# Kernel optimization log

Measured on AMD Instinct MI355X. Metric: run time of the kernel, lower is better.

The kernel has to match this reference:

```python
import jax, jax.numpy as jnp
import numpy as np

C = 32          # middle_channels
N_DOWN = 13     # layers 2..14, stride 2
DENSITY = 0.01  # nnz fraction of the 2048x2048 sparse matrix


def _conv(x, w):
    # centered SAME conv; inactive sites hold zeros so they contribute nothing,
    # matching MinkowskiConvolution's sum over existing neighbor coordinates.
    return jax.lax.conv_general_dilated(
        x, w, window_strides=(1, 1), padding='SAME',
        dimension_numbers=('NHWC', 'HWIO', 'NHWC'))


def _downsample_mask(mask):
    # ME stride-2 output coords = stride-quantized input coords -> OR over 2x2 block
    return jax.lax.reduce_window(mask, 0.0, jax.lax.max, (1, 2, 2), (1, 2, 2), 'SAME')


def _layer(x, mask, w, stride):
    y = _conv(x, w)
    if stride > 1:
        y = y[:, ::stride, ::stride, :]   # value at quantized coordinate u
        mask = _downsample_mask(mask)
    y = jax.nn.relu(y) * mask[..., None]  # ReLU on active sites, keep inactive = 0
    return y, mask


def _global_avg_pool(x, mask):
    cnt = jnp.maximum(jnp.sum(mask, axis=(1, 2)), 1.0)  # number of active coords
    return jnp.sum(x, axis=(1, 2)) / cnt[:, None]       # [B, C]


def setup_inputs() -> dict:
    key = jax.random.key(0)
    ks = jax.random.split(key, 8)
    H = W = 2048
    mask = (jax.random.uniform(ks[0], (1, H, W)) < DENSITY).astype(jnp.float32)
    x = jax.random.normal(ks[1], (1, H, W, 1), dtype=jnp.float32) * mask[..., None]
    # kaiming_normal fan_out (nonlinearity='relu') for conv kernels, bias=False in ME
    w1 = jax.random.normal(ks[2], (5, 5, 1, C), dtype=jnp.float32) * np.float32((2.0 / (5 * 5 * C)) ** 0.5)
    ws = jax.random.normal(ks[3], (N_DOWN, 3, 3, C, C), dtype=jnp.float32) * np.float32((2.0 / (3 * 3 * C)) ** 0.5)
    wm1 = jax.random.normal(ks[4], (C * 14, 256), dtype=jnp.float32) * np.float32((1.0 / (C * 14)) ** 0.5)
    bm1 = jnp.zeros((256,), jnp.float32)
    wm2 = jax.random.normal(ks[5], (256, 128), dtype=jnp.float32) * np.float32((1.0 / 256) ** 0.5)
    bm2 = jnp.zeros((128,), jnp.float32)
    return {'x': x, 'mask': mask, 'w1': w1, 'ws': ws,
            'wm1': wm1, 'bm1': bm1, 'wm2': wm2, 'bm2': bm2}


def reference(x, mask, w1, ws, wm1, bm1, wm2, bm2):
    y, m = _layer(x, mask, w1, stride=1)          # layer1: k=5, s=1
    pools = [_global_avg_pool(y, m)]
    for i in range(N_DOWN):                       # layers 2..14: k=3, s=2
        y, m = _layer(y, m, ws[i], stride=2)
        pools.append(_global_avg_pool(y, m))
    feat = jnp.concatenate(pools, axis=-1)        # [B, 32*14]
    h = jax.nn.relu(feat @ wm1 + bm1)
    return h @ wm2 + bm2                          # [B, 128]
```

## Files before the change

### kernel.cpp

```cpp
#include <hip/hip_runtime.h>

#define NLVL 14
#define NSHARD 16

struct ZeroArgs { unsigned long long zoff[13]; };

struct TailArgs {
    char* ws;
    const float* wm1; const float* bm1;
    const float* wm2; const float* bm2;
    float* out;
    unsigned long long idx8, idx9, idx10;
    unsigned long long nbr8, nbr9, nbr10;
    unsigned long long val7, val8, val9;
    int cap8, cap9, cap10;
};

__device__ __forceinline__ float fma4(float4 v, float4 w, float acc) {
    acc = fmaf(v.x, w.x, acc);
    acc = fmaf(v.y, w.y, acc);
    acc = fmaf(v.z, w.z, acc);
    return fmaf(v.w, w.w, acc);
}

__device__ __forceinline__ int cnt_load(const int* p) {
    return __hip_atomic_load(p, __ATOMIC_RELAXED, __HIP_MEMORY_SCOPE_AGENT);
}

#define GLDS16(gsrc, ldst) __builtin_amdgcn_global_load_lds( \
    (const __attribute__((address_space(1))) void*)(gsrc),   \
    (__attribute__((address_space(3))) void*)(ldst), 16, 0, 0)

__device__ __forceinline__ int block_scan_base(int mycnt, int* gcnt, int& myoff) {
    __shared__ int wsum[4];
    __shared__ int base;
    __syncthreads();
    int lane = threadIdx.x & 63, wid = threadIdx.x >> 6;
    int scan = mycnt;
    #pragma unroll
    for (int d = 1; d < 64; d <<= 1) {
        int tv = __shfl_up(scan, d, 64);
        if (lane >= d) scan += tv;
    }
    if (lane == 63) wsum[wid] = scan;
    __syncthreads();
    if (threadIdx.x == 0) {
        int tot = 0;
        #pragma unroll
        for (int i = 0; i < 4; i++) { int tv = wsum[i]; wsum[i] = tot; tot += tv; }
        base = tot ? atomicAdd(gcnt, tot) : 0;
    }
    __syncthreads();
    myoff = wsum[wid] + scan - mycnt;
    return base;
}

__device__ void compact0_tile(const float4* __restrict__ mask4, int* __restrict__ idxmap,
                              int* __restrict__ coords, int* __restrict__ cnt, int cap, int tile) {
    int t = threadIdx.x;
    int g0 = tile * 1024 + t;
    float4 m[4];
    #pragma unroll
    for (int j = 0; j < 4; j++) m[j] = mask4[g0 + j * 256];
    int pr[16];
    int mycnt = 0;
    #pragma unroll
    for (int j = 0; j < 4; j++) {
        pr[4 * j + 0] = m[j].x > 0.5f;
        pr[4 * j + 1] = m[j].y > 0.5f;
        pr[4 * j + 2] = m[j].z > 0.5f;
        pr[4 * j + 3] = m[j].w > 0.5f;
        mycnt += pr[4 * j] + pr[4 * j + 1] + pr[4 * j + 2] + pr[4 * j + 3];
    }
    int myoff;
    int base = block_scan_base(mycnt, cnt, myoff);
    int slot = base + myoff;
    #pragma unroll
    for (int j = 0; j < 4; j++) {
        int e0 = (g0 + j * 256) << 2;
        int wv[4];
        #pragma unroll
        for (int k = 0; k < 4; k++) {
            wv[k] = -1;
            if (pr[4 * j + k]) {
                int sl = slot++;
                if (sl < cap) { wv[k] = sl; coords[sl] = e0 + k; }
            }
        }
        *(int4*)(idxmap + e0) = make_int4(wv[0], wv[1], wv[2], wv[3]);
    }
}

__device__ void down_nbr(const int* __restrict__ idx_in, int HinB,
                         int* __restrict__ idx_out, int* __restrict__ nbr_out,
                         int* __restrict__ cnt_out, int HoutB, int cap_out,
                         int zofs, int bb) {
    int Hout = 1 << HoutB, Hin = 1 << HinB;
    int S = Hout * Hout;
    int S4 = (S + 3) >> 2;
    int o4 = bb * 256 + threadIdx.x;
    int e0 = o4 << 2;
    int jv[4][9];
    int pr[4] = {0, 0, 0, 0};
    #pragma unroll
    for (int k = 0; k < 4; k++)
        #pragma unroll
        for (int tap = 0; tap < 9; tap++) jv[k][tap] = -1;
    if (o4 < S4) {
        if (HoutB >= 2) {
            int r = e0 >> HoutB, c0 = e0 & (Hout - 1);
            int w[3][12];
            #pragma unroll
            for (int a = 0; a < 3; a++) {
                int rr = 2 * r + a - 1;
                bool rok = (unsigned)rr < (unsigned)Hin;
                const int* rowp = idx_in + ((size_t)(rok ? rr : 0) << HinB) + 2 * c0;
                int4 L = (rok && c0 > 0) ? *(const int4*)(rowp - 4) : make_int4(-1, -1, -1, -1);
                int4 M = rok ? *(const int4*)rowp : make_int4(-1, -1, -1, -1);
                int4 R = rok ? *(const int4*)(rowp + 4) : make_int4(-1, -1, -1, -1);
                w[a][0] = L.x; w[a][1] = L.y; w[a][2]  = L.z; w[a][3]  = L.w;
                w[a][4] = M.x; w[a][5] = M.y; w[a][6]  = M.z; w[a][7]  = M.w;
                w[a][8] = R.x; w[a][9] = R.y; w[a][10] = R.z; w[a][11] = R.w;
            }
            #pragma unroll
            for (int k = 0; k < 4; k++) {
                #pragma unroll
                for (int a = 0; a < 3; a++)
                    #pragma unroll
                    for (int b = 0; b < 3; b++)
                        jv[k][a * 3 + b] = w[a][2 * k + b + 3];
                pr[k] = ((jv[k][4] & jv[k][5] & jv[k][7] & jv[k][8]) >= 0);
            }
        } else {
            #pragma unroll
            for (int k = 0; k < 4; k++) {
                int p = e0 + k;
                if (p < S) {
                    int r = p >> HoutB, c = p & (Hout - 1);
                    #pragma unroll
                    for (int a = 0; a < 3; a++)
                        #pragma unroll
                        for (int b = 0; b < 3; b++) {
                            int rr = 2 * r + a - 1, cc = 2 * c + b - 1;
                            if ((unsigned)rr < (unsigned)Hin && (unsigned)cc < (unsigned)Hin)
                                jv[k][a * 3 + b] = idx_in[((size_t)rr << HinB) + cc];
                        }
                    pr[k] = ((jv[k][4] & jv[k][5] & jv[k][7] & jv[k][8]) >= 0);
                }
            }
        }
    }
    int mycnt = pr[0] + pr[1] + pr[2] + pr[3];
    int myoff;
    int base = block_scan_base(mycnt, cnt_out, myoff);
    int slot = base + myoff;
    int wv[4] = {-1, -1, -1, -1};
    #pragma unroll
    for (int k = 0; k < 4; k++) {
        if (pr[k]) {
            int sl = slot++;
            if (sl < cap_out) {
                wv[k] = sl;
                #pragma unroll
                for (int tap = 0; tap < 9; tap++) {
                    int j = jv[k][tap];
                    nbr_out[sl * 9 + tap] = (j < 0) ? zofs : (j << 7);
                }
            }
        }
    }
    if (o4 < S4) {
        if (S >= 4) *(int4*)(idx_out + e0) = make_int4(wv[0], wv[1], wv[2], wv[3]);
        else {
            #pragma unroll
            for (int k = 0; k < 4; k++) if (e0 + k < S) idx_out[e0 + k] = wv[k];
        }
    }
}

__device__ void down_small_wave(const int* __restrict__ idx_in, int HinB,
                                int* __restrict__ idx_out, int* __restrict__ nbr_out,
                                int* __restrict__ cnt_out, int HoutB, int cap_out,
                                int zofs) {
    int t = threadIdx.x;
    int Hout = 1 << HoutB, Hin = 1 << HinB, S = Hout * Hout;
    int p = t;
    int jv[9];
    int pr = 0;
    #pragma unroll
    for (int tap = 0; tap < 9; tap++) jv[tap] = -1;
    if (p < S) {
        int r = p >> HoutB, c = p & (Hout - 1);
        #pragma unroll
        for (int a = 0; a < 3; a++)
            #pragma unroll
            for (int b = 0; b < 3; b++) {
                int rr = 2 * r + a - 1, cc = 2 * c + b - 1;
                if ((unsigned)rr < (unsigned)Hin && (unsigned)cc < (unsigned)Hin)
                    jv[a * 3 + b] = idx_in[(rr << HinB) + cc];
            }
        pr = ((jv[4] & jv[5] & jv[7] & jv[8]) >= 0);
    }
    int scan = pr;
    #pragma unroll
    for (int d = 1; d < 64; d <<= 1) {
        int tv = __shfl_up(scan, d, 64);
        if (t >= d) scan += tv;
    }
    int myoff = scan - pr;
    int tot = __shfl(scan, 63, 64);
    if (p < S) {
        int wv = -1;
        if (pr && myoff < cap_out) {
            wv = myoff;
            #pragma unroll
            for (int tap = 0; tap < 9; tap++) {
                int j = jv[tap];
                nbr_out[myoff * 9 + tap] = (j < 0) ? zofs : (j << 7);
            }
        }
        idx_out[p] = wv;
    }
    if (t == 0 && tot) atomicAdd(cnt_out, tot);
}

__device__ void conv_small_1024(const char* __restrict__ vprevb,
                                const float* __restrict__ wlvl,
                                const int* __restrict__ nbr, int n,
                                float* __restrict__ vals, float* __restrict__ poolp) {
    __shared__ __align__(16) float s_in[576 * 32];
    int t = threadIdx.x;
    int ciq = t & 7, co = (t >> 3) & 31, sp = t >> 8;
    float4 wreg[9];
    #pragma unroll
    for (int tap = 0; tap < 9; tap++)
        wreg[tap] = *(const float4*)(wlvl + ((tap * 32 + co) << 5) + (ciq << 2));
    int items = n * 72;
    for (int i = t; i < items; i += 1024) {
        int row = i >> 3, q = i & 7;
        int jb = nbr[row];
        *(float4*)&s_in[(row << 5) + (q << 2)] =
            *(const float4*)(vprevb + jb + (q << 4));
    }
    __syncthreads();
    float ps = 0.f;
    #pragma unroll 1
    for (int gp = 0; gp < 16; gp++) {
        int g = gp * 4 + sp;
        if (g >= n) break;
        float a0 = 0.f;
        #pragma unroll
        for (int tap = 0; tap < 9; tap++) {
            float4 v = *(const float4*)&s_in[((g * 9 + tap) << 5) + (ciq << 2)];
            a0 = fma4(v, wreg[tap], a0);
        }
        a0 += __shfl_xor(a0, 1); a0 += __shfl_xor(a0, 2); a0 += __shfl_xor(a0, 4);
        if (ciq == 0) {
            float r0 = fmaxf(a0, 0.f);
            vals[((size_t)g << 5) + co] = r0;
            ps += r0;
        }
    }
    if (ciq == 0 && ps != 0.f) atomicAdd(&poolp[co], ps);
}

__device__ void conv_bs(const char* __restrict__ vprevb, const float* __restrict__ wlvl,
                        const int* __restrict__ nbr, int n,
                        float* __restrict__ vals, float* __restrict__ poolp,
                        int b0, int nbk, int shard) {
    __shared__ int s_j[2][144];
    __shared__ __align__(16) float s_in[2][144 * 32];
    int t = threadIdx.x;
    int ciq = t & 7, coh = (t >> 3) & 15, sp = t >> 7;
    int wid = t >> 6, lane = t & 63;
    float4 wreg[9][2];
    #pragma unroll
    for (int tap = 0; tap < 9; tap++) {
        wreg[tap][0] = *(const float4*)(wlvl + ((tap * 32 + coh) << 5) + (ciq << 2));
        wreg[tap][1] = *(const float4*)(wlvl + ((tap * 32 + coh + 16) << 5) + (ciq << 2));
    }
    float ps0 = 0.f, ps1 = 0.f;
    int ngr = (n + 15) >> 4;
    int n9 = n * 9;

    int jreg = 0;
    if (t < 144) {
        int gi = b0 * 144 + t;
        jreg = (b0 < ngr && gi < n9) ? nbr[gi] : 0;
        s_j[0][t] = jreg;
    }
    __syncthreads();
    if (b0 < ngr) {
        const int* sj = s_j[0];
        #pragma unroll
        for (int inst = 0; inst < 5; inst++) {
            int ii = wid + inst * 4;
            if (ii < 18) {
                int chunk = (ii << 6) + lane;
                int row = chunk >> 3, q = chunk & 7;
                GLDS16(vprevb + sj[row] + (q << 4), &s_in[0][ii << 8]);
            }
        }
    }
    if (t < 144) {
        int g1 = b0 + nbk;
        int gi = g1 * 144 + t;
        jreg = (g1 < ngr && gi < n9) ? nbr[gi] : 0;
    }

    int cur = 0;
    for (int grp = b0; grp < ngr; grp += nbk) {
        __syncthreads();
        bool hasnext = (grp + nbk) < ngr;
        if (t < 144) s_j[cur ^ 1][t] = jreg;
        __syncthreads();
        if (hasnext) {
            const int* sj = s_j[cur ^ 1];
            float* dst = s_in[cur ^ 1];
            #pragma unroll
            for (int inst = 0; inst < 5; inst++) {
                int ii = wid + inst * 4;
                if (ii < 18) {
                    int chunk = (ii << 6) + lane;
                    int row = chunk >> 3, q = chunk & 7;
                    GLDS16(vprevb + sj[row] + (q << 4), &dst[ii << 8]);
                }
            }
        }
        if (t < 144) {
            int g2 = grp + 2 * nbk;
            int gi = g2 * 144 + t;
            jreg = (g2 < ngr && gi < n9) ? nbr[gi] : 0;
        }
        const float* sb = s_in[cur];
        #pragma unroll
        for (int gp = 0; gp < 8; gp++) {
            int g = gp * 2 + sp;
            int s = (grp << 4) + g;
            float4 v[9];
            #pragma unroll
            for (int tap = 0; tap < 9; tap++)
                v[tap] = *(const float4*)&sb[((g * 9 + tap) << 5) + (ciq << 2)];
            float a0 = 0.f, a1 = 0.f;
            #pragma unroll
            for (int tap = 0; tap < 9; tap++) {
                a0 = fma4(v[tap], wreg[tap][0], a0);
                a1 = fma4(v[tap], wreg[tap][1], a1);
            }
            a0 += __shfl_xor(a0, 1); a0 += __shfl_xor(a0, 2); a0 += __shfl_xor(a0, 4);
            a1 += __shfl_xor(a1, 1); a1 += __shfl_xor(a1, 2); a1 += __shfl_xor(a1, 4);
            if (ciq == 0 && s < n) {
                float r0 = fmaxf(a0, 0.f), r1 = fmaxf(a1, 0.f);
                vals[((size_t)s << 5) + coh] = r0;
                vals[((size_t)s << 5) + coh + 16] = r1;
                ps0 += r0; ps1 += r1;
            }
        }
        cur ^= 1;
    }
    if (ciq == 0 && (ps0 != 0.f || ps1 != 0.f)) {
        atomicAdd(&poolp[shard * 448 + coh], ps0);
        atomicAdd(&poolp[shard * 448 + coh + 16], ps1);
    }
}

__device__ void conv0_bs(const float* __restrict__ x, const float* __restrict__ w1,
                         const int* __restrict__ coords0, int n,
                         float* __restrict__ vals0, float* __restrict__ poolp,
                         int b0, int nbk, int shard) {
    __shared__ float lw[800];
    __shared__ float lx[8][28];
    __shared__ float red[256];
    int t = threadIdx.x;
    for (int i = t; i < 800; i += 256) lw[i] = w1[i];
    int sl = t >> 5, ch = t & 31;
    float psum = 0.f;
    int ngr = (n + 7) >> 3;
    for (int grp = b0; grp < ngr; grp += nbk) {
        __syncthreads();
        if (t < 200) {
            int slot = t / 25, tap = t - slot * 25;
            int s = (grp << 3) + slot;
            float v = 0.f;
            if (s < n) {
                int p = coords0[s];
                int r = p >> 11, c = p & 2047;
                int a = tap / 5, b = tap - a * 5;
                int rr = r + a - 2, cc = c + b - 2;
                if ((unsigned)rr < 2048u && (unsigned)cc < 2048u)
                    v = x[(rr << 11) + cc];
            }
            lx[slot][tap] = v;
        }
        __syncthreads();
        int s = (grp << 3) + sl;
        float acc = 0.f;
        #pragma unroll
        for (int tap = 0; tap < 25; tap++)
            acc = fmaf(lx[sl][tap], lw[tap * 32 + ch], acc);
        if (s < n) {
            float r0 = fmaxf(acc, 0.f);
            vals0[((size_t)s << 5) + ch] = r0;
            psum += r0;
        }
    }
    __syncthreads();
    red[t] = psum;
    __syncthreads();
    if (t < 32) {
        float tot = 0.f;
        #pragma unroll
        for (int q = 0; q < 8; q++) tot += red[t + 32 * q];
        if (tot != 0.f) atomicAdd(&poolp[shard * 448 + t], tot);
    }
}

__global__ __launch_bounds__(256) void k_f0(
    const float4* __restrict__ mask4, int* __restrict__ idxmap,
    int* __restrict__ coords, int* __restrict__ cnt, int cap,
    const float* __restrict__ w, float* __restrict__ wt,
    char* __restrict__ wsbase, ZeroArgs za) {
    if (blockIdx.x == 1492) {
        for (int i = threadIdx.x; i < 13 * 32; i += 256)
            *(float*)(wsbase + za.zoff[i >> 5] + ((i & 31) << 2)) = 0.f;
        return;
    }
    if (blockIdx.x >= 1024) {
        int t = (int)(blockIdx.x - 1024) * 256 + threadIdx.x;
        if (t < 13 * 9 * 32 * 32) {
            int ci = t & 31, co = (t >> 5) & 31, tp = t >> 10;
            wt[(tp << 10) + (co << 5) + ci] = w[(tp << 10) + (ci << 5) + co];
        }
        return;
    }
    compact0_tile(mask4, idxmap, coords, cnt, cap, blockIdx.x);
}

__global__ __launch_bounds__(256) void k_f1(
    const int* __restrict__ idx0, int* __restrict__ idx1, int* __restrict__ nbr1,
    int* __restrict__ cnt1, int cap1, int zofs1,
    const float* __restrict__ x, const float* __restrict__ w1,
    const int* __restrict__ coords0, const int* __restrict__ cnt0, int cap0,
    float* __restrict__ vals0, float* __restrict__ poolp,
    const float* __restrict__ wm1, const float* __restrict__ wm2, float* __restrict__ dummy) {
    if (blockIdx.x < 1024) {
        down_nbr(idx0, 11, idx1, nbr1, cnt1, 10, cap1, zofs1, blockIdx.x);
        return;
    }
    if (blockIdx.x >= 5120) {
        int t = (int)(blockIdx.x - 5120) * 256 + threadIdx.x;
        const float4* a = (const float4*)wm1;
        const float4* b = (const float4*)wm2;
        float acc = 0.f;
        for (int i = t; i < 28672; i += 6144) { float4 v = a[i]; acc += v.x + v.y + v.z + v.w; }
        for (int i = t; i < 8192; i += 6144)  { float4 v = b[i]; acc += v.x + v.y + v.z + v.w; }
        if (acc == 1234.56789f) dummy[0] = acc;
        return;
    }
    int n = *cnt0; if (n > cap0) n = cap0;
    conv0_bs(x, w1, coords0, n, vals0, poolp, blockIdx.x - 1024, 4096, blockIdx.x & (NSHARD - 1));
}

__global__ __launch_bounds__(256) void k_flevel(
    int downB,
    const int* __restrict__ idx_in, int HinB,
    int* __restrict__ idx_out, int* __restrict__ nbr_out, int* __restrict__ cnt_out,
    int HoutB, int cap_out, int zofs,
    const char* __restrict__ vprevb, const float* __restrict__ wlvl,
    const int* __restrict__ nbr_c, const int* __restrict__ cnt_c, int cap_c,
    float* __restrict__ vals_c, float* __restrict__ poolp) {
    if ((int)blockIdx.x < downB) {
        down_nbr(idx_in, HinB, idx_out, nbr_out, cnt_out, HoutB, cap_out, zofs, blockIdx.x);
        return;
    }
    int n = *cnt_c; if (n > cap_c) n = cap_c;
    conv_bs(vprevb, wlvl, nbr_c, n, vals_c, poolp,
            blockIdx.x - downB, gridDim.x - downB, blockIdx.x & (NSHARD - 1));
}

__global__ __launch_bounds__(1024) void k_tail3(TailArgs a) {
    char* ws = a.ws;
    int* cnt = (int*)ws;
    float* poolsh = (float*)(ws + 256);
    float* wt = (float*)(ws + 32768);
    int t = threadIdx.x;

    if (t < 64)
        down_small_wave((const int*)(ws + a.idx8), 3, (int*)(ws + a.idx9),
                        (int*)(ws + a.nbr9), cnt + 9, 2, a.cap9, a.cap8 * 128);
    __syncthreads();
    {
        int n8 = cnt_load(cnt + 8); if (n8 > a.cap8) n8 = a.cap8;
        conv_small_1024((const char*)(ws + a.val7), wt + (size_t)7 * 9216,
                        (const int*)(ws + a.nbr8), n8,
                        (float*)(ws + a.val8), poolsh + 8 * 32);
    }
    __syncthreads();
    if (t < 64)
        down_small_wave((const int*)(ws + a.idx9), 2, (int*)(ws + a.idx10),
                        (int*)(ws + a.nbr10), cnt + 10, 1, a.cap10, a.cap9 * 128);
    __syncthreads();
    {
        int n9 = cnt_load(cnt + 9); if (n9 > a.cap9) n9 = a.cap9;
        conv_small_1024((const char*)(ws + a.val8), wt + (size_t)8 * 9216,
                        (const int*)(ws + a.nbr9), n9,
                        (float*)(ws + a.val9), poolsh + 9 * 32);
    }
    __syncthreads();

    const char* vals9b = (const char*)(ws + a.val9);
    const int* nbr10 = (const int*)(ws + a.nbr10);
    const int* idx10 = (const int*)(ws + a.idx10);
    __shared__ __align__(16) float v10[128];
    __shared__ float v11[32], v12[32], v13[32];
    __shared__ float feat[448], h[256], part[1024];
    __shared__ int s_i10[4], s_n10;
    int ciq = t & 7, co = (t >> 3) & 31, s = t >> 8;
    int ciq16 = ciq << 4;
    if (t == 0) s_n10 = cnt_load(cnt + 10);
    if (t < 4) s_i10[t] = idx10[t];
    __syncthreads();
    int n10 = s_n10; if (n10 > 4) n10 = 4;
    {
        const float* wl = wt + (size_t)9 * 9216;
        float4 wreg[9];
        #pragma unroll
        for (int tap = 0; tap < 9; tap++)
            wreg[tap] = *(const float4*)(wl + ((tap * 32 + co) << 5) + (ciq << 2));
        bool live = s < n10;
        int sb = live ? s : 0;
        float a0 = 0.f;
        #pragma unroll
        for (int tap = 0; tap < 9; tap++)
            a0 = fma4(*(const float4*)(vals9b + nbr10[sb * 9 + tap] + ciq16), wreg[tap], a0);
        a0 += __shfl_xor(a0, 1); a0 += __shfl_xor(a0, 2); a0 += __shfl_xor(a0, 4);
        if (ciq == 0 && live) v10[s * 32 + co] = fmaxf(a0, 0.f);
    }
    __syncthreads();
    int i10[4] = {s_i10[0], s_i10[1], s_i10[2], s_i10[3]};
    int nbr11[9];
    #pragma unroll
    for (int tap = 0; tap < 9; tap++) {
        int aa = tap / 3, bb = tap - aa * 3;
        int rr = aa - 1, cc = bb - 1;
        nbr11[tap] = ((unsigned)rr < 2u && (unsigned)cc < 2u) ? i10[rr * 2 + cc] : -1;
    }
    int n11 = ((nbr11[4] & nbr11[5] & nbr11[7] & nbr11[8]) >= 0) ? 1 : 0;
    if (s == 0) {
        const float* wl = wt + (size_t)10 * 9216;
        float a0 = 0.f;
        #pragma unroll
        for (int tap = 0; tap < 9; tap++) {
            int j = nbr11[tap];
            if (j >= 0) {
                float4 wv = *(const float4*)(wl + ((tap * 32 + co) << 5) + (ciq << 2));
                a0 = fma4(*(const float4*)(&v10[(j << 5) + (ciq << 2)]), wv, a0);
            }
        }
        a0 += __shfl_xor(a0, 1); a0 += __shfl_xor(a0, 2); a0 += __shfl_xor(a0, 4);
        if (ciq == 0) v11[co] = n11 ? fmaxf(a0, 0.f) : 0.f;
    }
    __syncthreads();
    if (s == 0) {
        const float* wl = wt + (size_t)11 * 9216;
        float4 wv = *(const float4*)(wl + ((4 * 32 + co) << 5) + (ciq << 2));
        float a0 = n11 ? fma4(*(const float4*)(&v11[ciq << 2]), wv, 0.f) : 0.f;
        a0 += __shfl_xor(a0, 1); a0 += __shfl_xor(a0, 2); a0 += __shfl_xor(a0, 4);
        if (ciq == 0) v12[co] = n11 ? fmaxf(a0, 0.f) : 0.f;
    }
    __syncthreads();
    if (s == 0) {
        const float* wl = wt + (size_t)12 * 9216;
        float4 wv = *(const float4*)(wl + ((4 * 32 + co) << 5) + (ciq << 2));
        float a0 = n11 ? fma4(*(const float4*)(&v12[ciq << 2]), wv, 0.f) : 0.f;
        a0 += __shfl_xor(a0, 1); a0 += __shfl_xor(a0, 2); a0 += __shfl_xor(a0, 4);
        if (ciq == 0) v13[co] = n11 ? fmaxf(a0, 0.f) : 0.f;
    }
    __syncthreads();
    if (t < 320) {
        float sum = 0.f;
        #pragma unroll
        for (int sh = 0; sh < NSHARD; sh++) sum += poolsh[sh * 448 + t];
        float c = (float)cnt_load(cnt + (t >> 5)); if (c < 1.f) c = 1.f;
        feat[t] = sum / c;
    }
    if (t < 32) {
        float s10 = 0.f;
        for (int q = 0; q < n10; q++) s10 += v10[q * 32 + t];
        float c10 = (float)n10; if (c10 < 1.f) c10 = 1.f;
        feat[320 + t] = s10 / c10;
        feat[352 + t] = n11 ? v11[t] : 0.f;
        feat[384 + t] = n11 ? v12[t] : 0.f;
        feat[416 + t] = n11 ? v13[t] : 0.f;
    }
    __syncthreads();
    {
        int j = t & 255, chunk = t >> 8;
        float acc = (chunk == 0) ? a.bm1[j] : 0.f;
        int k0 = chunk * 112;
        #pragma unroll 8
        for (int k = k0; k < k0 + 112; k++) acc = fmaf(feat[k], a.wm1[k * 256 + j], acc);
        part[t] = acc;
    }
    __syncthreads();
    if (t < 256)
        h[t] = fmaxf(part[t] + part[t + 256] + part[t + 512] + part[t + 768], 0.f);
    __syncthreads();
    {
        int j2 = t & 127, c2 = t >> 7;
        float a2 = (c2 == 0) ? a.bm2[j2] : 0.f;
        int kk0 = c2 * 32;
        #pragma unroll 8
        for (int k = kk0; k < kk0 + 32; k++) a2 = fmaf(h[k], a.wm2[k * 128 + j2], a2);
        part[t] = a2;
    }
    __syncthreads();
    if (t < 128) {
        float sum = 0.f;
        #pragma unroll
        for (int c = 0; c < 8; c++) sum += part[t + 128 * c];
        a.out[t] = sum;
    }
}

extern "C" void kernel_launch(void* const* d_in, const int* in_sizes, int n_in,
                              void* d_out, int out_size, void* d_ws, size_t ws_size,
                              hipStream_t stream) {
    const float* x    = (const float*)d_in[0];
    const float* mask = (const float*)d_in[1];
    const float* w1   = (const float*)d_in[2];
    const float* wsrc = (const float*)d_in[3];
    const float* wm1  = (const float*)d_in[4];
    const float* bm1  = (const float*)d_in[5];
    const float* wm2  = (const float*)d_in[6];
    const float* bm2  = (const float*)d_in[7];
    float* out = (float*)d_out;
    char* ws = (char*)d_ws;

    static const int Hb[NLVL]   = {11, 10, 9, 8, 7, 6, 5, 4, 3, 2, 1, 0, 0, 0};
    static const int caps[NLVL] = {45056, 43008, 43008, 34816, 16384, 4096,
                                   1024, 256, 64, 16, 4, 1, 1, 1};

    size_t pool_off = 256;
    size_t wt_off = 32768;
    size_t off = wt_off + (size_t)13 * 9 * 1024 * 4;
    off = (off + 255) & ~(size_t)255;
    size_t coord0_off = off; off += (size_t)caps[0] * 4; off = (off + 255) & ~(size_t)255;
    size_t idx_off[NLVL], nbr_off[NLVL], val_off[NLVL];
    for (int l = 0; l < NLVL; l++) {
        size_t S = (size_t)(1 << Hb[l]) * (1 << Hb[l]);
        size_t sb = S * 4; if (sb < 16) sb = 16;
        idx_off[l] = off; off += sb; off = (off + 255) & ~(size_t)255;
        if (l >= 1) { nbr_off[l] = off; off += (size_t)caps[l] * 36; off = (off + 255) & ~(size_t)255; }
        else nbr_off[l] = 0;
        val_off[l] = off; off += (size_t)(caps[l] + 1) * 128; off = (off + 255) & ~(size_t)255;
    }

    int* cnt = (int*)ws;
    float* poolsh = (float*)(ws + pool_off);
    float* dummy = (float*)(ws + 128);
    float* wt = (float*)(ws + wt_off);

    ZeroArgs za;
    for (int l = 0; l < 13; l++) za.zoff[l] = val_off[l] + (size_t)caps[l] * 128;

    hipMemsetAsync(ws, 0, 32768, stream);

    k_f0<<<1493, 256, 0, stream>>>(
        (const float4*)mask, (int*)(ws + idx_off[0]), (int*)(ws + coord0_off),
        cnt, caps[0], wsrc, wt, ws, za);

    k_f1<<<5144, 256, 0, stream>>>(
        (const int*)(ws + idx_off[0]), (int*)(ws + idx_off[1]), (int*)(ws + nbr_off[1]),
        cnt + 1, caps[1], caps[0] * 128,
        x, w1, (const int*)(ws + coord0_off), cnt, caps[0],
        (float*)(ws + val_off[0]), poolsh, wm1, wm2, dummy);

    for (int i = 2; i <= 8; i++) {
        int lc = i - 1;
        int Hout = 1 << Hb[i];
        int S4 = (Hout * Hout + 3) >> 2;
        int downB = (S4 + 255) >> 8; if (downB < 1) downB = 1;
        int convB = (caps[lc] + 15) >> 4;
        if (convB > 768) convB = 768;
        k_flevel<<<downB + convB, 256, 0, stream>>>(
            downB,
            (const int*)(ws + idx_off[i - 1]), Hb[i - 1],
            (int*)(ws + idx_off[i]), (int*)(ws + nbr_off[i]), cnt + i, Hb[i], caps[i],
            caps[i - 1] * 128,
            (const char*)(ws + val_off[lc - 1]), wt + (size_t)(lc - 1) * 9216,
            (const int*)(ws + nbr_off[lc]), cnt + lc, caps[lc],
            (float*)(ws + val_off[lc]), poolsh + lc * 32);
    }

    TailArgs ta;
    ta.ws = ws;
    ta.wm1 = wm1; ta.bm1 = bm1; ta.wm2 = wm2; ta.bm2 = bm2;
    ta.out = out;
    ta.idx8 = idx_off[8];  ta.idx9 = idx_off[9];  ta.idx10 = idx_off[10];
    ta.nbr8 = nbr_off[8];  ta.nbr9 = nbr_off[9];  ta.nbr10 = nbr_off[10];
    ta.val7 = val_off[7];  ta.val8 = val_off[8];  ta.val9 = val_off[9];
    ta.cap8 = caps[8]; ta.cap9 = caps[9]; ta.cap10 = caps[10];
    k_tail3<<<1, 1024, 0, stream>>>(ta);
}
```

Measured before the change: 244.1 us.

## Fold level-7 conv into single-block tail kernel and prefetch neighbor indices in registers

Cuts the multi-block per-level launch loop one level earlier and moves that level's downsample and conv into the single 1024-thread tail kernel. To support this, conv_small_1024 now processes active sites in chunks of 64, so it can handle counts larger than its shared buffer. Separately, conv_bs drops the shared-memory staging of neighbor indices and its extra barrier, and each thread loads the indices it needs straight into registers for the async global-to-LDS copies. The trade-off is that a larger level now runs on one block with serialized chunks, in exchange for one fewer kernel launch and fewer syncs.

```diff
diff --git a/kernel.cpp b/kernel.cpp
--- a/kernel.cpp
+++ b/kernel.cpp
@@ -10,10 +10,10 @@
     const float* wm1; const float* bm1;
     const float* wm2; const float* bm2;
     float* out;
-    unsigned long long idx8, idx9, idx10;
-    unsigned long long nbr8, nbr9, nbr10;
-    unsigned long long val7, val8, val9;
-    int cap8, cap9, cap10;
+    unsigned long long idx7, idx8, idx9, idx10;
+    unsigned long long nbr7, nbr8, nbr9, nbr10;
+    unsigned long long val6, val7, val8, val9;
+    int cap7, cap8, cap9, cap10;
 };
 
 __device__ __forceinline__ float fma4(float4 v, float4 w, float acc) {
@@ -235,30 +235,34 @@
     #pragma unroll
     for (int tap = 0; tap < 9; tap++)
         wreg[tap] = *(const float4*)(wlvl + ((tap * 32 + co) << 5) + (ciq << 2));
-    int items = n * 72;
-    for (int i = t; i < items; i += 1024) {
-        int row = i >> 3, q = i & 7;
-        int jb = nbr[row];
-        *(float4*)&s_in[(row << 5) + (q << 2)] =
-            *(const float4*)(vprevb + jb + (q << 4));
-    }
-    __syncthreads();
     float ps = 0.f;
-    #pragma unroll 1
-    for (int gp = 0; gp < 16; gp++) {
-        int g = gp * 4 + sp;
-        if (g >= n) break;
-        float a0 = 0.f;
-        #pragma unroll
-        for (int tap = 0; tap < 9; tap++) {
-            float4 v = *(const float4*)&s_in[((g * 9 + tap) << 5) + (ciq << 2)];
-            a0 = fma4(v, wreg[tap], a0);
-        }
-        a0 += __shfl_xor(a0, 1); a0 += __shfl_xor(a0, 2); a0 += __shfl_xor(a0, 4);
-        if (ciq == 0) {
-            float r0 = fmaxf(a0, 0.f);
-            vals[((size_t)g << 5) + co] = r0;
-            ps += r0;
+    for (int c0 = 0; c0 < n; c0 += 64) {
+        int nc = n - c0; if (nc > 64) nc = 64;
+        __syncthreads();
+        int items = nc * 72;
+        for (int i = t; i < items; i += 1024) {
+            int row = i >> 3, q = i & 7;
+            int jb = nbr[c0 * 9 + row];
+            *(float4*)&s_in[(row << 5) + (q << 2)] =
+                *(const float4*)(vprevb + jb + (q << 4));
+        }
+        __syncthreads();
+        #pragma unroll 1
+        for (int gp = 0; gp < 16; gp++) {
+            int g = gp * 4 + sp;
+            if (g >= nc) break;
+            float a0 = 0.f;
+            #pragma unroll
+            for (int tap = 0; tap < 9; tap++) {
+                float4 v = *(const float4*)&s_in[((g * 9 + tap) << 5) + (ciq << 2)];
+                a0 = fma4(v, wreg[tap], a0);
+            }
+            a0 += __shfl_xor(a0, 1); a0 += __shfl_xor(a0, 2); a0 += __shfl_xor(a0, 4);
+            if (ciq == 0) {
+                float r0 = fmaxf(a0, 0.f);
+                vals[((size_t)(c0 + g) << 5) + co] = r0;
+                ps += r0;
+            }
         }
     }
     if (ciq == 0 && ps != 0.f) atomicAdd(&poolp[co], ps);
@@ -268,11 +272,10 @@
                         const int* __restrict__ nbr, int n,
                         float* __restrict__ vals, float* __restrict__ poolp,
                         int b0, int nbk, int shard) {
-    __shared__ int s_j[2][144];
     __shared__ __align__(16) float s_in[2][144 * 32];
     int t = threadIdx.x;
     int ciq = t & 7, coh = (t >> 3) & 15, sp = t >> 7;
-    int wid = t >> 6, lane = t & 63;
+    int wid = t >> 6, lrow = (t >> 3) & 7, lq = t & 7;
     float4 wreg[9][2];
     #pragma unroll
     for (int tap = 0; tap < 9; tap++) {
@@ -283,54 +286,51 @@
     int ngr = (n + 15) >> 4;
     int n9 = n * 9;
 
-    int jreg = 0;
-    if (t < 144) {
-        int gi = b0 * 144 + t;
-        jreg = (b0 < ngr && gi < n9) ? nbr[gi] : 0;
-        s_j[0][t] = jreg;
-    }
-    __syncthreads();
+    int jn[5];
+    #pragma unroll
+    for (int inst = 0; inst < 5; inst++) {
+        int ii = wid + inst * 4;
+        int gi = b0 * 144 + ii * 8 + lrow;
+        jn[inst] = (b0 < ngr && ii < 18 && gi < n9) ? nbr[gi] : 0;
+    }
     if (b0 < ngr) {
-        const int* sj = s_j[0];
         #pragma unroll
         for (int inst = 0; inst < 5; inst++) {
             int ii = wid + inst * 4;
-            if (ii < 18) {
-                int chunk = (ii << 6) + lane;
-                int row = chunk >> 3, q = chunk & 7;
-                GLDS16(vprevb + sj[row] + (q << 4), &s_in[0][ii << 8]);
-            }
-        }
-    }
-    if (t < 144) {
+            if (ii < 18)
+                GLDS16(vprevb + jn[inst] + (lq << 4), &s_in[0][ii << 8]);
+        }
+    }
+    {
         int g1 = b0 + nbk;
-        int gi = g1 * 144 + t;
-        jreg = (g1 < ngr && gi < n9) ? nbr[gi] : 0;
+        #pragma unroll
+        for (int inst = 0; inst < 5; inst++) {
+            int ii = wid + inst * 4;
+            int gi = g1 * 144 + ii * 8 + lrow;
+            jn[inst] = (g1 < ngr && ii < 18 && gi < n9) ? nbr[gi] : 0;
+        }
     }
 
     int cur = 0;
     for (int grp = b0; grp < ngr; grp += nbk) {
         __syncthreads();
-        bool hasnext = (grp + nbk) < ngr;
-        if (t < 144) s_j[cur ^ 1][t] = jreg;
-        __syncthreads();
-        if (hasnext) {
-            const int* sj = s_j[cur ^ 1];
+        if (grp + nbk < ngr) {
             float* dst = s_in[cur ^ 1];
             #pragma unroll
             for (int inst = 0; inst < 5; inst++) {
                 int ii = wid + inst * 4;
-                if (ii < 18) {
-                    int chunk = (ii << 6) + lane;
-                    int row = chunk >> 3, q = chunk & 7;
-                    GLDS16(vprevb + sj[row] + (q << 4), &dst[ii << 8]);
-                }
-            }
-        }
-        if (t < 144) {
+                if (ii < 18)
+                    GLDS16(vprevb + jn[inst] + (lq << 4), &dst[ii << 8]);
+            }
+        }
+        {
             int g2 = grp + 2 * nbk;
-            int gi = g2 * 144 + t;
-            jreg = (g2 < ngr && gi < n9) ? nbr[gi] : 0;
+            #pragma unroll
+            for (int inst = 0; inst < 5; inst++) {
+                int ii = wid + inst * 4;
+                int gi = g2 * 144 + ii * 8 + lrow;
+                jn[inst] = (g2 < ngr && ii < 18 && gi < n9) ? nbr[gi] : 0;
+            }
         }
         const float* sb = s_in[cur];
         #pragma unroll
@@ -478,13 +478,24 @@
             blockIdx.x - downB, gridDim.x - downB, blockIdx.x & (NSHARD - 1));
 }
 
-__global__ __launch_bounds__(1024) void k_tail3(TailArgs a) {
+__global__ __launch_bounds__(1024) void k_tail4(TailArgs a) {
     char* ws = a.ws;
     int* cnt = (int*)ws;
     float* poolsh = (float*)(ws + 256);
     float* wt = (float*)(ws + 32768);
     int t = threadIdx.x;
 
+    if (t < 64)
+        down_small_wave((const int*)(ws + a.idx7), 4, (int*)(ws + a.idx8),
+                        (int*)(ws + a.nbr8), cnt + 8, 3, a.cap8, a.cap7 * 128);
+    __syncthreads();
+    {
+        int n7 = cnt_load(cnt + 7); if (n7 > a.cap7) n7 = a.cap7;
+        conv_small_1024((const char*)(ws + a.val6), wt + (size_t)6 * 9216,
+                        (const int*)(ws + a.nbr7), n7,
+                        (float*)(ws + a.val7), poolsh + 7 * 32);
+    }
+    __syncthreads();
     if (t < 64)
         down_small_wave((const int*)(ws + a.idx8), 3, (int*)(ws + a.idx9),
                         (int*)(ws + a.nbr9), cnt + 9, 2, a.cap9, a.cap8 * 128);
@@ -676,7 +687,7 @@
         x, w1, (const int*)(ws + coord0_off), cnt, caps[0],
         (float*)(ws + val_off[0]), poolsh, wm1, wm2, dummy);
 
-    for (int i = 2; i <= 8; i++) {
+    for (int i = 2; i <= 7; i++) {
         int lc = i - 1;
         int Hout = 1 << Hb[i];
         int S4 = (Hout * Hout + 3) >> 2;
@@ -697,9 +708,12 @@
     ta.ws = ws;
     ta.wm1 = wm1; ta.bm1 = bm1; ta.wm2 = wm2; ta.bm2 = bm2;
     ta.out = out;
-    ta.idx8 = idx_off[8];  ta.idx9 = idx_off[9];  ta.idx10 = idx_off[10];
-    ta.nbr8 = nbr_off[8];  ta.nbr9 = nbr_off[9];  ta.nbr10 = nbr_off[10];
-    ta.val7 = val_off[7];  ta.val8 = val_off[8];  ta.val9 = val_off[9];
-    ta.cap8 = caps[8]; ta.cap9 = caps[9]; ta.cap10 = caps[10];
-    k_tail3<<<1, 1024, 0, stream>>>(ta);
-}
+    ta.idx7 = idx_off[7];  ta.idx8 = idx_off[8];
+    ta.idx9 = idx_off[9];  ta.idx10 = idx_off[10];
+    ta.nbr7 = nbr_off[7];  ta.nbr8 = nbr_off[8];
+    ta.nbr9 = nbr_off[9];  ta.nbr10 = nbr_off[10];
+    ta.val6 = val_off[6];  ta.val7 = val_off[7];
+    ta.val8 = val_off[8];  ta.val9 = val_off[9];
+    ta.cap7 = caps[7]; ta.cap8 = caps[8]; ta.cap9 = caps[9]; ta.cap10 = caps[10];
+    k_tail4<<<1, 1024, 0, stream>>>(ta);
+}
```

Result: slower. 285.7 us (+17.0%).
